# Kernel optimization log

Measured on AMD Instinct MI355X. Metric: run time of the kernel, lower is better.

The kernel has to match this reference:

```python
import jax, jax.numpy as jnp
import numpy as np

B, T, S, D, H = 16, 2048, 2048, 1024, 24  # batch, text len, encoded len, feature dim, head dim


def setup_inputs() -> dict:
    key = jax.random.key(0)
    ks = jax.random.split(key, 6)
    return {
        "encoded": jax.random.normal(ks[0], (B, S, D), dtype=jnp.float32),
        "text": jax.random.normal(ks[1], (B, T, D), dtype=jnp.float32),
        "wq": jax.random.normal(ks[2], (D, H), dtype=jnp.float32) * 0.02,
        "wk": jax.random.normal(ks[3], (D, H), dtype=jnp.float32) * 0.02,
        "wv": jax.random.normal(ks[4], (D, H), dtype=jnp.float32) * 0.02,
        "wh": jax.random.normal(ks[5], (H, D), dtype=jnp.float32) * 0.02,
    }


def reference(encoded, text, wq, wk, wv, wh):
    q = text @ wq          # [B, T, H]
    k = encoded @ wk       # [B, S, H]
    v = encoded @ wv       # [B, S, H]
    a = jnp.einsum("bth,bsh->bts", q, k)   # [B, T, S]
    # NOTE: original applies softmax over dim=1 (the QUERY axis), not the key axis.
    a = jax.nn.softmax(a, axis=1)
    h1 = jnp.einsum("bts,bsh->bth", a, v)  # [B, T, H]
    return h1 @ wh         # [B, T, D]
```

## Files before the change

### kernel.cpp

```cpp
#include <hip/hip_runtime.h>
#include <hip/hip_bf16.h>

#define B_ 16
#define T_ 2048
#define S_ 2048
#define D_ 1024
#define H_ 24
#define NROW_ (B_ * T_)
#define BS_ (B_ * S_)
#define QN32_ ((size_t)NROW_ * 32)

typedef float f32x16 __attribute__((ext_vector_type(16)));
typedef __bf16 bf16x8 __attribute__((ext_vector_type(8)));

union B8u { int4 i; bf16x8 b; };
__device__ inline bf16x8 pun(int4 v) { B8u u; u.i = v; return u.b; }

__device__ inline ushort f2bf(float f) {
  uint u = __float_as_uint(f);
  u += 0x7fffu + ((u >> 16) & 1u);
  return (ushort)(u >> 16);
}
__device__ inline float bf2f(ushort u) { return __uint_as_float(((uint)u) << 16); }

__device__ inline f32x16 mfma32(bf16x8 a, bf16x8 b, f32x16 c) {
  return __builtin_amdgcn_mfma_f32_32x32x16_bf16(a, b, c, 0, 0, 0);
}

__device__ inline uint cvtpk(float a, float b) {
  uint r;
  asm("v_cvt_pk_bf16_f32 %0, %1, %2" : "=v"(r) : "v"(a), "v"(b));
  return r;
}

#define AS1C(p) ((const __attribute__((address_space(1))) void*)((const void*)(p)))
#define AS3(p) ((__attribute__((address_space(3))) void*)((void*)(p)))

__global__ __launch_bounds__(256) void prep_w(
    const float* __restrict__ wq, const float* __restrict__ wk,
    const float* __restrict__ wv, ushort* __restrict__ wpk) {
  int i = blockIdx.x * 256 + threadIdx.x;
  if (i >= 3 * 128 * H_) return;
  int which = i / (128 * H_);
  int rem = i - which * 128 * H_;
  int k8g = rem / H_, n = rem - k8g * H_;
  const float* w = (which == 0) ? wq : (which == 1) ? wk : wv;
  ushort t[8];
#pragma unroll
  for (int j = 0; j < 8; ++j) t[j] = f2bf(w[(k8g * 8 + j) * H_ + n]);
  *(int4*)&wpk[(size_t)i * 8] = *(const int4*)t;
}

__global__ __launch_bounds__(256, 2) void proj_unified(
    const float* __restrict__ text, const float* __restrict__ encoded,
    const ushort* __restrict__ wpk, ushort* __restrict__ qb,
    ushort* __restrict__ kbuf, float* __restrict__ vv) {
  __shared__ __align__(16) float sA[4][2][2048];

  const int tid = threadIdx.x;
  const int lane = tid & 63, lo = lane & 31, hi = lane >> 5, w = tid >> 6;
  const bool kvmode = (blockIdx.x >= 1024);
  const int bid = kvmode ? (blockIdx.x - 1024) : blockIdx.x;
  const float* in = kvmode ? encoded : text;
  const ushort* wp1 = wpk + (size_t)(kvmode ? 1 : 0) * 128 * H_ * 8;
  const ushort* wp2 = wpk + (size_t)2 * 128 * H_ * 8;
  const long rowbase = (long)bid * 32;
  const int ne = (lo < H_) ? lo : 0;

  int4 bfr1[16], bfr2[16];
#pragma unroll
  for (int win = 0; win < 4; ++win) {
#pragma unroll
    for (int cl = 0; cl < 4; ++cl) {
      const int k8g = w * 32 + win * 8 + 2 * cl + hi;
      bfr1[win * 4 + cl] = *(const int4*)&wp1[(size_t)(k8g * H_ + ne) * 8];
      if (kvmode)
        bfr2[win * 4 + cl] = *(const int4*)&wp2[(size_t)(k8g * H_ + ne) * 8];
    }
  }

  const int srow = lane >> 4;
  const int c16l = lane & 15;
  const float* gbase = in + rowbase * D_ + w * 256;

  f32x16 acc = {};
  f32x16 acc2 = {};

#define STAGE(win_, buf_)                                                     \
  {                                                                           \
    _Pragma("unroll") for (int i = 0; i < 8; ++i) {                           \
      const int row = i * 4 + srow;                                           \
      const int c16s = c16l ^ ((row & 7) << 1);      \
      const float* g = gbase + (size_t)row * D_ + (win_)*64 + c16s * 4;       \
      __builtin_amdgcn_global_load_lds(AS1C(g), AS3(&sA[w][buf_][i * 256]),   \
                                       16, 0, 0);                             \
    }                                                                         \
  }

  STAGE(0, 0);
#pragma unroll
  for (int win = 0; win < 4; ++win) {
    const int buf = win & 1;
    __builtin_amdgcn_sched_barrier(0);
    if (win < 3) {
      if (win == 0) STAGE(1, 1);
      if (win == 1) STAGE(2, 0);
      if (win == 2) STAGE(3, 1);
      asm volatile("s_waitcnt vmcnt(8)" ::: "memory");
    } else {
      asm volatile("s_waitcnt vmcnt(0)" ::: "memory");
    }
    __builtin_amdgcn_sched_barrier(0);
#pragma unroll
    for (int cl = 0; cl < 4; ++cl) {
      const int k8 = 2 * cl + hi;
      const int c16 = (2 * k8) ^ ((lo & 7) << 1);
      float4 ga = *(const float4*)&sA[w][buf][lo * 64 + c16 * 4];
      float4 gb = *(const float4*)&sA[w][buf][lo * 64 + c16 * 4 + 4];
      uint p0 = cvtpk(ga.x, ga.y), p1 = cvtpk(ga.z, ga.w);
      uint p2 = cvtpk(gb.x, gb.y), p3 = cvtpk(gb.z, gb.w);
      bf16x8 a = pun(make_int4(p0, p1, p2, p3));
      acc = mfma32(a, pun(bfr1[win * 4 + cl]), acc);
      if (kvmode) acc2 = mfma32(a, pun(bfr2[win * 4 + cl]), acc2);
    }
  }
#undef STAGE

  float* sR = (float*)sA;
  __syncthreads();
#pragma unroll
  for (int r = 0; r < 16; ++r) sR[w * 1088 + lane * 17 + r] = acc[r];
  __syncthreads();
  {
    const int qd = tid >> 6, l = tid & 63, lo2 = l & 31, hi2 = l >> 5;
    ushort* o1 = (kvmode ? kbuf : qb);
#pragma unroll
    for (int rr = 0; rr < 4; ++rr) {
      const int r = qd * 4 + rr;
      float s = sR[0 * 1088 + l * 17 + r] + sR[1 * 1088 + l * 17 + r] +
                sR[2 * 1088 + l * 17 + r] + sR[3 * 1088 + l * 17 + r];
      const int mrow = rr + 8 * qd + 4 * hi2;
      o1[(size_t)(rowbase + mrow) * 32 + lo2] = (lo2 < H_) ? f2bf(s) : (ushort)0;
    }
  }
  if (kvmode) {
    __syncthreads();
#pragma unroll
    for (int r = 0; r < 16; ++r) sR[w * 1088 + lane * 17 + r] = acc2[r];
    __syncthreads();
    const int qd = tid >> 6, l = tid & 63, lo2 = l & 31, hi2 = l >> 5;
    if (lo2 < H_) {
#pragma unroll
      for (int rr = 0; rr < 4; ++rr) {
        const int r = qd * 4 + rr;
        float s = sR[0 * 1088 + l * 17 + r] + sR[1 * 1088 + l * 17 + r] +
                  sR[2 * 1088 + l * 17 + r] + sR[3 * 1088 + l * 17 + r];
        const int mrow = rr + 8 * qd + 4 * hi2;
        vv[(size_t)(rowbase + mrow) * H_ + lo2] = s;
      }
    }
  }
}

__global__ __launch_bounds__(256) void colsum_mfma(
    const ushort* __restrict__ qb, const ushort* __restrict__ kb,
    float* __restrict__ dpart) {
  __shared__ __align__(16) ushort sQ[4 * 32 * 8];
  const int tid = threadIdx.x;
  const int lane = tid & 63;
  const int lo = lane & 31, hi = lane >> 5;
  const int w = tid >> 6;
  const int b = blockIdx.y;
  const int s0 = blockIdx.x * 128 + w * 32;
  const int tpart = blockIdx.z;

  const ushort* krow = kb + ((size_t)b * S_ + s0 + lo) * 32;
  bf16x8 k0 = pun(*(const int4*)(krow + hi * 8));
  bf16x8 k1 = pun(*(const int4*)(krow + 16 + hi * 8));

  float dl = 0.f;
  for (int tc = 0; tc < 16; ++tc) {
    const int tbase = tpart * 512 + tc * 32;
    if (tid < 128) {
      int t = tid >> 2, j = tid & 3;
      *(int4*)&sQ[j * 256 + t * 8] =
          *(const int4*)(qb + ((size_t)b * T_ + tbase + t) * 32 + j * 8);
    }
    __syncthreads();
    bf16x8 qa = pun(*(const int4*)&sQ[hi * 256 + lo * 8]);
    bf16x8 qc = pun(*(const int4*)&sQ[(2 + hi) * 256 + lo * 8]);
    f32x16 c = {};
    c = mfma32(qa, k0, c);
    c = mfma32(qc, k1, c);
#pragma unroll
    for (int r = 0; r < 16; ++r) dl += __expf(c[r]);
    __syncthreads();
  }
  dl += __shfl_xor(dl, 32);
  if (hi == 0) dpart[(size_t)tpart * BS_ + (size_t)b * S_ + s0 + lo] = dl;
}

__global__ __launch_bounds__(256) void vscale_kernel(
    const float* __restrict__ vv, const float* __restrict__ dpart,
    ushort* __restrict__ vsT) {
  int gid = blockIdx.x * 256 + threadIdx.x;
  int s4 = gid & 511;
  int h = (gid >> 9) & 31;
  int b = gid >> 14;
  int s0 = s4 * 4;
  ushort4 ov;
  if (h < H_) {
    const float* vp = vv + ((size_t)b * S_ + s0) * H_ + h;
    const float* dp = dpart + (size_t)b * S_ + s0;
    float dv[4];
#pragma unroll
    for (int i = 0; i < 4; ++i) {
      float d = dp[i] + dp[BS_ + i] + dp[2 * BS_ + i] + dp[3 * BS_ + i];
      dv[i] = 1.0f / d;
    }
    ov.x = f2bf(vp[0 * H_] * dv[0]);
    ov.y = f2bf(vp[1 * H_] * dv[1]);
    ov.z = f2bf(vp[2 * H_] * dv[2]);
    ov.w = f2bf(vp[3 * H_] * dv[3]);
  } else {
    ov.x = ov.y = ov.z = ov.w = 0;
  }
  *(ushort4*)&vsT[((size_t)b * 32 + h) * S_ + s0] = ov;
}

__global__ __launch_bounds__(256) void attn_mfma(
    const ushort* __restrict__ qb, const ushort* __restrict__ kb,
    const ushort* __restrict__ vsT, ushort* __restrict__ h1p) {
  __shared__ __align__(16) ushort sK[4 * 32 * 8];
  __shared__ __align__(16) ushort sV[4 * 32 * 8];
  const int tid = threadIdx.x;
  const int lane = tid & 63;
  const int lo = lane & 31, hi = lane >> 5;
  const int w = tid >> 6;
  const int b = blockIdx.y;
  const int t0 = blockIdx.x * 128 + w * 32;
  const int spart = blockIdx.z;

  const ushort* qrow = qb + ((size_t)b * T_ + t0 + lo) * 32;
  bf16x8 q0 = pun(*(const int4*)(qrow + hi * 8));
  bf16x8 q1 = pun(*(const int4*)(qrow + 16 + hi * 8));

  f32x16 hacc = {};
  for (int sc = 0; sc < 16; ++sc) {
    const int sbase = spart * 512 + sc * 32;
    if (tid < 128) {
      int s = tid >> 2, j = tid & 3;
      *(int4*)&sK[j * 256 + s * 8] =
          *(const int4*)(kb + ((size_t)b * S_ + sbase + s) * 32 + j * 8);
    } else {
      int i2 = tid - 128;
      int h = i2 >> 2, q = i2 & 3;
      *(int4*)&sV[q * 256 + h * 8] =
          *(const int4*)(vsT + ((size_t)b * 32 + h) * S_ + sbase + q * 8);
    }
    __syncthreads();
    bf16x8 ka = pun(*(const int4*)&sK[hi * 256 + lo * 8]);
    bf16x8 kc = pun(*(const int4*)&sK[(2 + hi) * 256 + lo * 8]);
    bf16x8 va = pun(*(const int4*)&sV[hi * 256 + lo * 8]);
    bf16x8 vc = pun(*(const int4*)&sV[(2 + hi) * 256 + lo * 8]);
    f32x16 c = {};
    c = mfma32(ka, q0, c);
    c = mfma32(kc, q1, c);
    uint pk[8];
#pragma unroll
    for (int m = 0; m < 8; ++m) {
      float plo = __expf(c[2 * m]);
      float phi = __expf(c[2 * m + 1]);
      pk[m] = cvtpk(plo, phi);
    }
    asm("v_permlane32_swap_b32 %0, %1" : "+v"(pk[0]), "+v"(pk[2]));
    asm("v_permlane32_swap_b32 %0, %1" : "+v"(pk[1]), "+v"(pk[3]));
    asm("v_permlane32_swap_b32 %0, %1" : "+v"(pk[4]), "+v"(pk[6]));
    asm("v_permlane32_swap_b32 %0, %1" : "+v"(pk[5]), "+v"(pk[7]));
    int4 f0 = make_int4(pk[0], pk[1], pk[2], pk[3]);
    int4 f1 = make_int4(pk[4], pk[5], pk[6], pk[7]);
    hacc = mfma32(pun(f0), va, hacc);
    hacc = mfma32(pun(f1), vc, hacc);
    __syncthreads();
  }
  ushort* o = h1p + (size_t)spart * QN32_ + (size_t)b * T_ * 32;
#pragma unroll
  for (int r = 0; r < 16; ++r) {
    int trow = t0 + (r & 3) + 8 * (r >> 2) + 4 * hi;
    o[(size_t)trow * 32 + lo] = f2bf(hacc[r]);
  }
}

__global__ __launch_bounds__(256) void out_kernel(const ushort* __restrict__ h1p,
                                                  const float* __restrict__ wh,
                                                  float* __restrict__ out) {
  __shared__ __align__(16) float s_h1[16 * 24];
  const int tid = threadIdx.x;
  const long rbase = (long)blockIdx.x * 16;
  if (tid < 48) {
    const int r = tid / 3, c8 = tid - 3 * r;
    float s[8] = {0.f, 0.f, 0.f, 0.f, 0.f, 0.f, 0.f, 0.f};
#pragma unroll
    for (int part = 0; part < 4; ++part) {
      int4 v = *(const int4*)&h1p[(size_t)part * QN32_ +
                                  (size_t)(rbase + r) * 32 + c8 * 8];
      const ushort* u = (const ushort*)&v;
#pragma unroll
      for (int j = 0; j < 8; ++j) s[j] += bf2f(u[j]);
    }
#pragma unroll
    for (int j = 0; j < 8; ++j) s_h1[r * 24 + c8 * 8 + j] = s[j];
  }
  __syncthreads();
  for (int c = 0; c < 4; ++c) {
    const int dd = c * 256 + tid;
    float wr[24];
#pragma unroll
    for (int h = 0; h < 24; ++h) wr[h] = wh[h * D_ + dd];
#pragma unroll 1
    for (int r = 0; r < 16; ++r) {
      float a = 0.f;
#pragma unroll
      for (int j = 0; j < 6; ++j) {
        float4 hv = *(const float4*)(s_h1 + r * 24 + 4 * j);
        a = fmaf(hv.x, wr[4 * j], a);
        a = fmaf(hv.y, wr[4 * j + 1], a);
        a = fmaf(hv.z, wr[4 * j + 2], a);
        a = fmaf(hv.w, wr[4 * j + 3], a);
      }
      out[(rbase + r) * D_ + dd] = a;
    }
  }
}

extern "C" void kernel_launch(void* const* d_in, const int* in_sizes, int n_in,
                              void* d_out, int out_size, void* d_ws,
                              size_t ws_size, hipStream_t stream) {
  const float* encoded = (const float*)d_in[0];
  const float* text = (const float*)d_in[1];
  const float* wq = (const float*)d_in[2];
  const float* wk = (const float*)d_in[3];
  const float* wv = (const float*)d_in[4];
  const float* wh = (const float*)d_in[5];
  float* out = (float*)d_out;

  ushort* qb = (ushort*)d_ws;
  ushort* kbuf = qb + QN32_;
  float* vv = (float*)(kbuf + QN32_);
  float* dpart = vv + (size_t)BS_ * H_;
  ushort* vsT = (ushort*)(dpart + 4 * BS_);
  ushort* h1p = vsT + (size_t)B_ * 32 * S_;
  ushort* wpk = h1p + 4 * QN32_;

  prep_w<<<36, 256, 0, stream>>>(wq, wk, wv, wpk);
  proj_unified<<<2048, 256, 0, stream>>>(text, encoded, wpk, qb, kbuf, vv);
  colsum_mfma<<<dim3(S_ / 128, B_, 4), 256, 0, stream>>>(qb, kbuf, dpart);
  vscale_kernel<<<(B_ * 32 * (S_ / 4)) / 256, 256, 0, stream>>>(vv, dpart, vsT);
  attn_mfma<<<dim3(T_ / 128, B_, 4), 256, 0, stream>>>(qb, kbuf, vsT, h1p);
  out_kernel<<<NROW_ / 16, 256, 0, stream>>>(h1p, wh, out);
}
```

Measured before the change: 156.5 us.

## Split unified projection into separate Q and KV kernels with smaller staging tiles

Replaces the single projection kernel, which branched on block index between Q and KV modes, with two kernels. proj_q uses 256 threads with 32-column windows, halving LDS per block so more blocks fit per CU. proj_kv uses 512 threads (8 waves, each covering 128 of the D columns) so its doubled MFMA work is spread across more waves, and it reduces partial sums over 8 waves. The aim is to remove the load imbalance and register pressure of the unified kernel and raise occupancy. The cost is an extra launch, a serial dependency between the two launches, and a larger cross-wave reduction in proj_kv.

```diff
diff --git a/kernel.cpp b/kernel.cpp
--- a/kernel.cpp
+++ b/kernel.cpp
@@ -51,80 +51,148 @@
   *(int4*)&wpk[(size_t)i * 8] = *(const int4*)t;
 }
 
-__global__ __launch_bounds__(256, 2) void proj_unified(
-    const float* __restrict__ text, const float* __restrict__ encoded,
-    const ushort* __restrict__ wpk, ushort* __restrict__ qb,
-    ushort* __restrict__ kbuf, float* __restrict__ vv) {
-  __shared__ __align__(16) float sA[4][2][2048];
+
+__global__ __launch_bounds__(256, 4) void proj_q(
+    const float* __restrict__ in, const ushort* __restrict__ wpk,
+    ushort* __restrict__ qb) {
+  __shared__ __align__(16) float sA[4][2][1024];
 
   const int tid = threadIdx.x;
   const int lane = tid & 63, lo = lane & 31, hi = lane >> 5, w = tid >> 6;
-  const bool kvmode = (blockIdx.x >= 1024);
-  const int bid = kvmode ? (blockIdx.x - 1024) : blockIdx.x;
-  const float* in = kvmode ? encoded : text;
-  const ushort* wp1 = wpk + (size_t)(kvmode ? 1 : 0) * 128 * H_ * 8;
-  const ushort* wp2 = wpk + (size_t)2 * 128 * H_ * 8;
-  const long rowbase = (long)bid * 32;
+  const long rowbase = (long)blockIdx.x * 32;
   const int ne = (lo < H_) ? lo : 0;
 
-  int4 bfr1[16], bfr2[16];
-#pragma unroll
-  for (int win = 0; win < 4; ++win) {
-#pragma unroll
-    for (int cl = 0; cl < 4; ++cl) {
-      const int k8g = w * 32 + win * 8 + 2 * cl + hi;
-      bfr1[win * 4 + cl] = *(const int4*)&wp1[(size_t)(k8g * H_ + ne) * 8];
-      if (kvmode)
-        bfr2[win * 4 + cl] = *(const int4*)&wp2[(size_t)(k8g * H_ + ne) * 8];
-    }
-  }
-
-  const int srow = lane >> 4;
-  const int c16l = lane & 15;
+  int4 bfr[16];
+#pragma unroll
+  for (int win = 0; win < 8; ++win)
+#pragma unroll
+    for (int cl = 0; cl < 2; ++cl) {
+      const int k8g = w * 32 + win * 4 + 2 * cl + hi;
+      bfr[win * 2 + cl] = *(const int4*)&wpk[(size_t)(k8g * H_ + ne) * 8];
+    }
+
+  const int srow8 = lane >> 3;
+  const int gq = lane & 7;
   const float* gbase = in + rowbase * D_ + w * 256;
 
-  f32x16 acc = {};
-  f32x16 acc2 = {};
-
-#define STAGE(win_, buf_)                                                     \
+#define STAGE_Q(win_, buf_)                                                   \
   {                                                                           \
-    _Pragma("unroll") for (int i = 0; i < 8; ++i) {                           \
-      const int row = i * 4 + srow;                                           \
-      const int c16s = c16l ^ ((row & 7) << 1);      \
-      const float* g = gbase + (size_t)row * D_ + (win_)*64 + c16s * 4;       \
+    _Pragma("unroll") for (int i = 0; i < 4; ++i) {                           \
+      const int row = i * 8 + srow8;                                          \
+      const int sg = gq ^ ((row & 3) << 1);                                   \
+      const float* g = gbase + (size_t)row * D_ + (win_) * 32 + sg * 4;       \
       __builtin_amdgcn_global_load_lds(AS1C(g), AS3(&sA[w][buf_][i * 256]),   \
                                        16, 0, 0);                             \
     }                                                                         \
   }
 
-  STAGE(0, 0);
+  f32x16 acc = {};
+  const int rbs = (lo >> 3) * 256 + (lo & 7) * 32;
+
+  STAGE_Q(0, 0);
+#pragma unroll
+  for (int win = 0; win < 8; ++win) {
+    const int buf = win & 1;
+    if (win < 7) {
+      STAGE_Q(win + 1, buf ^ 1);
+      asm volatile("s_waitcnt vmcnt(4)" ::: "memory");
+    } else {
+      asm volatile("s_waitcnt vmcnt(0)" ::: "memory");
+    }
+    __builtin_amdgcn_sched_barrier(0);
+#pragma unroll
+    for (int cl = 0; cl < 2; ++cl) {
+      const int pg = (4 * cl + 2 * hi) ^ ((lo & 3) << 1);
+      float4 fa = *(const float4*)&sA[w][buf][rbs + pg * 4];
+      float4 fb = *(const float4*)&sA[w][buf][rbs + pg * 4 + 4];
+      uint p0 = cvtpk(fa.x, fa.y), p1 = cvtpk(fa.z, fa.w);
+      uint p2 = cvtpk(fb.x, fb.y), p3 = cvtpk(fb.z, fb.w);
+      acc = mfma32(pun(make_int4(p0, p1, p2, p3)), pun(bfr[win * 2 + cl]), acc);
+    }
+  }
+#undef STAGE_Q
+
+  float* sR = (float*)sA;
+  __syncthreads();
+#pragma unroll
+  for (int r = 0; r < 16; ++r) sR[w * 1088 + lane * 17 + r] = acc[r];
+  __syncthreads();
+  const int qd = tid >> 6, l = tid & 63, lo2 = l & 31, hi2 = l >> 5;
+#pragma unroll
+  for (int rr = 0; rr < 4; ++rr) {
+    const int r = qd * 4 + rr;
+    float s = sR[0 * 1088 + l * 17 + r] + sR[1 * 1088 + l * 17 + r] +
+              sR[2 * 1088 + l * 17 + r] + sR[3 * 1088 + l * 17 + r];
+    const int mrow = rr + 8 * qd + 4 * hi2;
+    qb[(size_t)(rowbase + mrow) * 32 + lo2] = (lo2 < H_) ? f2bf(s) : (ushort)0;
+  }
+}
+
+__global__ __launch_bounds__(512, 4) void proj_kv(
+    const float* __restrict__ in, const ushort* __restrict__ wpk,
+    ushort* __restrict__ kbuf, float* __restrict__ vv) {
+  __shared__ __align__(16) float sA[8][2][1024];
+
+  const int tid = threadIdx.x;
+  const int lane = tid & 63, lo = lane & 31, hi = lane >> 5, w = tid >> 6;
+  const long rowbase = (long)blockIdx.x * 32;
+  const int ne = (lo < H_) ? lo : 0;
+  const ushort* wp1 = wpk + (size_t)1 * 128 * H_ * 8;
+  const ushort* wp2 = wpk + (size_t)2 * 128 * H_ * 8;
+
+  int4 bfr1[8], bfr2[8];
+#pragma unroll
+  for (int win = 0; win < 4; ++win)
+#pragma unroll
+    for (int cl = 0; cl < 2; ++cl) {
+      const int k8g = w * 16 + win * 4 + 2 * cl + hi;
+      bfr1[win * 2 + cl] = *(const int4*)&wp1[(size_t)(k8g * H_ + ne) * 8];
+      bfr2[win * 2 + cl] = *(const int4*)&wp2[(size_t)(k8g * H_ + ne) * 8];
+    }
+
+  const int srow8 = lane >> 3;
+  const int gq = lane & 7;
+  const float* gbase = in + rowbase * D_ + w * 128;
+
+#define STAGE_KV(win_, buf_)                                                  \
+  {                                                                           \
+    _Pragma("unroll") for (int i = 0; i < 4; ++i) {                           \
+      const int row = i * 8 + srow8;                                          \
+      const int sg = gq ^ ((row & 3) << 1);                                   \
+      const float* g = gbase + (size_t)row * D_ + (win_) * 32 + sg * 4;       \
+      __builtin_amdgcn_global_load_lds(AS1C(g), AS3(&sA[w][buf_][i * 256]),   \
+                                       16, 0, 0);                             \
+    }                                                                         \
+  }
+
+  f32x16 acc = {};
+  f32x16 acc2 = {};
+  const int rbs = (lo >> 3) * 256 + (lo & 7) * 32;
+
+  STAGE_KV(0, 0);
 #pragma unroll
   for (int win = 0; win < 4; ++win) {
     const int buf = win & 1;
-    __builtin_amdgcn_sched_barrier(0);
     if (win < 3) {
-      if (win == 0) STAGE(1, 1);
-      if (win == 1) STAGE(2, 0);
-      if (win == 2) STAGE(3, 1);
-      asm volatile("s_waitcnt vmcnt(8)" ::: "memory");
+      STAGE_KV(win + 1, buf ^ 1);
+      asm volatile("s_waitcnt vmcnt(4)" ::: "memory");
     } else {
       asm volatile("s_waitcnt vmcnt(0)" ::: "memory");
     }
     __builtin_amdgcn_sched_barrier(0);
 #pragma unroll
-    for (int cl = 0; cl < 4; ++cl) {
-      const int k8 = 2 * cl + hi;
-      const int c16 = (2 * k8) ^ ((lo & 7) << 1);
-      float4 ga = *(const float4*)&sA[w][buf][lo * 64 + c16 * 4];
-      float4 gb = *(const float4*)&sA[w][buf][lo * 64 + c16 * 4 + 4];
-      uint p0 = cvtpk(ga.x, ga.y), p1 = cvtpk(ga.z, ga.w);
-      uint p2 = cvtpk(gb.x, gb.y), p3 = cvtpk(gb.z, gb.w);
+    for (int cl = 0; cl < 2; ++cl) {
+      const int pg = (4 * cl + 2 * hi) ^ ((lo & 3) << 1);
+      float4 fa = *(const float4*)&sA[w][buf][rbs + pg * 4];
+      float4 fb = *(const float4*)&sA[w][buf][rbs + pg * 4 + 4];
+      uint p0 = cvtpk(fa.x, fa.y), p1 = cvtpk(fa.z, fa.w);
+      uint p2 = cvtpk(fb.x, fb.y), p3 = cvtpk(fb.z, fb.w);
       bf16x8 a = pun(make_int4(p0, p1, p2, p3));
-      acc = mfma32(a, pun(bfr1[win * 4 + cl]), acc);
-      if (kvmode) acc2 = mfma32(a, pun(bfr2[win * 4 + cl]), acc2);
-    }
-  }
-#undef STAGE
+      acc = mfma32(a, pun(bfr1[win * 2 + cl]), acc);
+      acc2 = mfma32(a, pun(bfr2[win * 2 + cl]), acc2);
+    }
+  }
+#undef STAGE_KV
 
   float* sR = (float*)sA;
   __syncthreads();
@@ -132,29 +200,35 @@
   for (int r = 0; r < 16; ++r) sR[w * 1088 + lane * 17 + r] = acc[r];
   __syncthreads();
   {
-    const int qd = tid >> 6, l = tid & 63, lo2 = l & 31, hi2 = l >> 5;
-    ushort* o1 = (kvmode ? kbuf : qb);
-#pragma unroll
-    for (int rr = 0; rr < 4; ++rr) {
+    const int q8 = tid >> 6, l = tid & 63, lo2 = l & 31, hi2 = l >> 5;
+    const int qd = q8 & 3, half = q8 >> 2;
+#pragma unroll
+    for (int rr2 = 0; rr2 < 2; ++rr2) {
+      const int rr = half * 2 + rr2;
       const int r = qd * 4 + rr;
-      float s = sR[0 * 1088 + l * 17 + r] + sR[1 * 1088 + l * 17 + r] +
-                sR[2 * 1088 + l * 17 + r] + sR[3 * 1088 + l * 17 + r];
+      float s = 0.f;
+#pragma unroll
+      for (int ww = 0; ww < 8; ++ww) s += sR[ww * 1088 + l * 17 + r];
       const int mrow = rr + 8 * qd + 4 * hi2;
-      o1[(size_t)(rowbase + mrow) * 32 + lo2] = (lo2 < H_) ? f2bf(s) : (ushort)0;
-    }
-  }
-  if (kvmode) {
-    __syncthreads();
-#pragma unroll
-    for (int r = 0; r < 16; ++r) sR[w * 1088 + lane * 17 + r] = acc2[r];
-    __syncthreads();
-    const int qd = tid >> 6, l = tid & 63, lo2 = l & 31, hi2 = l >> 5;
+      kbuf[(size_t)(rowbase + mrow) * 32 + lo2] =
+          (lo2 < H_) ? f2bf(s) : (ushort)0;
+    }
+  }
+  __syncthreads();
+#pragma unroll
+  for (int r = 0; r < 16; ++r) sR[w * 1088 + lane * 17 + r] = acc2[r];
+  __syncthreads();
+  {
+    const int q8 = tid >> 6, l = tid & 63, lo2 = l & 31, hi2 = l >> 5;
+    const int qd = q8 & 3, half = q8 >> 2;
     if (lo2 < H_) {
 #pragma unroll
-      for (int rr = 0; rr < 4; ++rr) {
+      for (int rr2 = 0; rr2 < 2; ++rr2) {
+        const int rr = half * 2 + rr2;
         const int r = qd * 4 + rr;
-        float s = sR[0 * 1088 + l * 17 + r] + sR[1 * 1088 + l * 17 + r] +
-                  sR[2 * 1088 + l * 17 + r] + sR[3 * 1088 + l * 17 + r];
+        float s = 0.f;
+#pragma unroll
+        for (int ww = 0; ww < 8; ++ww) s += sR[ww * 1088 + l * 17 + r];
         const int mrow = rr + 8 * qd + 4 * hi2;
         vv[(size_t)(rowbase + mrow) * H_ + lo2] = s;
       }
@@ -353,7 +427,8 @@
   ushort* wpk = h1p + 4 * QN32_;
 
   prep_w<<<36, 256, 0, stream>>>(wq, wk, wv, wpk);
-  proj_unified<<<2048, 256, 0, stream>>>(text, encoded, wpk, qb, kbuf, vv);
+  proj_q<<<1024, 256, 0, stream>>>(text, wpk, qb);
+  proj_kv<<<1024, 512, 0, stream>>>(encoded, wpk, kbuf, vv);
   colsum_mfma<<<dim3(S_ / 128, B_, 4), 256, 0, stream>>>(qb, kbuf, dpart);
   vscale_kernel<<<(B_ * 32 * (S_ / 4)) / 256, 256, 0, stream>>>(vv, dpart, vsT);
   attn_mfma<<<dim3(T_ / 128, B_, 4), 256, 0, stream>>>(qb, kbuf, vsT, h1p);
```

Measured after the change: 161.2 us. +2.9%, slower.
